# Kernel optimization log

Hardware: AMD Instinct MI355X
Metric: run time of the kernel (lower is better)

The kernel has to match this reference:

```python
import jax, jax.numpy as jnp
import numpy as np
from jax import lax

INF = 1e10
R = 20          # max_distance: EDT truncated at this radius (exact under clamp)
NUM_CLASSES = 19


def _pass1d(f, axis):
    """1D squared distance transform min_{|d|<=R} (d^2 + f[shifted]), truncated.
    f: [..., H, W] with 0 at 'source' pixels, INF elsewhere. Out-of-bounds = INF
    (matches scipy, which sees nothing beyond the array border)."""
    pad = [(0, 0)] * f.ndim
    pad[axis] = (R, R)
    fp = jnp.pad(f, pad, constant_values=INF)
    n = f.shape[axis]
    out = jnp.full_like(f, INF)
    for d in range(2 * R + 1):  # fixed small loop (41 iters), jit-unrolled
        shifted = lax.slice_in_dim(fp, d, d + n, axis=axis)
        out = jnp.minimum(out, shifted + float((d - R) ** 2))
    return out


def edt_trunc(mask):
    """Euclidean distance from each True pixel to nearest False pixel,
    truncated at R (False pixels get 0). mask: [..., H, W] bool."""
    f = jnp.where(mask, INF, 0.0).astype(jnp.float32)
    g = _pass1d(f, -2)
    g = _pass1d(g, -1)
    return jnp.sqrt(jnp.minimum(g, float(R * R)))


def compute_sdf(onehot_bool):
    """Signed distance: negdist - posdist, per [B,C,H,W] one-hot masks.
    Already truncated at +-R, matching clamp(-R, R) in the torch module."""
    posdist = edt_trunc(onehot_bool)    # distance inside FG to BG
    negdist = edt_trunc(~onehot_bool)   # distance inside BG to FG
    return negdist - posdist


def setup_inputs() -> dict:
    key = jax.random.key(0)
    k1, k2 = jax.random.split(key)
    logits = jax.random.normal(k1, (8, NUM_CLASSES, 256, 512), dtype=jnp.float32)
    targets = jax.random.randint(k2, (8, 256, 512), 0, NUM_CLASSES, dtype=jnp.int64)
    return {"logits": logits, "targets": targets}


def reference(logits, targets):
    C = logits.shape[1]
    probs = jax.nn.softmax(logits, axis=1)                       # [B,C,H,W]
    onehot = jax.nn.one_hot(targets, C, axis=1, dtype=jnp.bool_)  # [B,C,H,W]
    sdf = compute_sdf(onehot)
    sdf = jnp.clip(sdf, -float(R), float(R)) / float(R)
    # mean over spatial, sum over classes, mean over batch (reduction='mean')
    per_class = jnp.mean(probs * sdf, axis=(2, 3))               # [B,C]
    loss = jnp.sum(per_class, axis=1)                            # [B]
    return jnp.mean(loss)
```

## Files before the change

### kernel.cpp

```cpp
#include <hip/hip_runtime.h>
#include <hip/hip_bf16.h>
#include <math.h>

#define NCLS 19
#define BB   8
#define HH   256
#define WW   512
#define CAP2 400u
#define SEG  8
#define WPC  70

typedef unsigned short u16x2 __attribute__((ext_vector_type(2)));

static __device__ __forceinline__ unsigned umin32(unsigned a, unsigned b) { return a < b ? a : b; }
static __device__ __forceinline__ float fsqrt_fast(float x) { return __builtin_amdgcn_sqrtf(x); }

static __device__ __forceinline__ unsigned pk_add_s(unsigned v, unsigned c) {
    unsigned d; asm("v_pk_add_u16 %0, %1, %2" : "=v"(d) : "s"(c), "v"(v)); return d;
}
static __device__ __forceinline__ unsigned pk_minv(unsigned a, unsigned b) {
    unsigned d; asm("v_pk_min_u16 %0, %1, %2" : "=v"(d) : "v"(a), "v"(b)); return d;
}
static __device__ __forceinline__ unsigned pk_maxv(unsigned a, unsigned b) {
    unsigned d; asm("v_pk_max_u16 %0, %1, %2" : "=v"(d) : "v"(a), "v"(b)); return d;
}
static __device__ __forceinline__ unsigned pk_hmin(unsigned a) {
    unsigned d;
    asm("v_pk_min_u16 %0, %1, %1 op_sel:[1,0] op_sel_hi:[0,1]" : "=v"(d) : "v"(a));
    return d;
}
static __device__ __forceinline__ void sq8(unsigned x, unsigned& w0, unsigned& w1) {
    unsigned a = x & 0x00FF00FFu;
    unsigned b = (x >> 8) & 0x00FF00FFu;
    u16x2 sa = __builtin_bit_cast(u16x2, a); sa = sa * sa;
    u16x2 sb = __builtin_bit_cast(u16x2, b); sb = sb * sb;
    unsigned ua = __builtin_bit_cast(unsigned, sa);
    unsigned ub = __builtin_bit_cast(unsigned, sb);
    w0 = __builtin_amdgcn_perm(ub, ua, 0x05040100u);
    w1 = __builtin_amdgcn_perm(ub, ua, 0x07060302u);
}

__global__ __launch_bounds__(256)
void kA_vert(const int* __restrict__ targ, unsigned char* __restrict__ vneg,
             unsigned long long* __restrict__ acc) {
    if (blockIdx.x == 0 && threadIdx.x < 64) acc[threadIdx.x] = 0ULL;
    int gid = blockIdx.x * 256 + threadIdx.x;
    int col = gid & 4095;
    int seg = gid >> 12;
    int b = col >> 9;
    int w = col & 511;
    int h0 = seg * SEG;
    const int* tp = &targ[b * HH * WW + w];

    unsigned d[NCLS];
    unsigned pk[NCLS][2];
#pragma unroll
    for (int c = 0; c < NCLS; ++c) { d[c] = 21u; pk[c][0] = 0u; pk[c][1] = 0u; }
#pragma unroll
    for (int k = 0; k < 21 + SEG; ++k) {
        int hh = h0 - 21 + k;
        int t = -1;
        if (hh >= 0) t = tp[hh * WW];
#pragma unroll
        for (int c = 0; c < NCLS; ++c)
            d[c] = (t == c) ? 0u : d[c] + 1u;
        if (k >= 21) {
            int r = k - 21;
#pragma unroll
            for (int c = 0; c < NCLS; ++c)
                pk[c][r >> 2] |= d[c] << ((r & 3) * 8);
        }
    }
    unsigned u[NCLS];
#pragma unroll
    for (int c = 0; c < NCLS; ++c) u[c] = 21u;
#pragma unroll
    for (int k = 0; k < 21 + SEG; ++k) {
        int hh = h0 + 21 + SEG - 1 - k;
        int t = -1;
        if (hh < HH) t = tp[hh * WW];
#pragma unroll
        for (int c = 0; c < NCLS; ++c)
            u[c] = (t == c) ? 0u : u[c] + 1u;
        if (k >= 21) {
            int r = 21 + SEG - 1 - k;
#pragma unroll
            for (int c = 0; c < NCLS; ++c) {
                unsigned dv = (pk[c][r >> 2] >> ((r & 3) * 8)) & 0xffu;
                vneg[((size_t)(b * NCLS + c) * HH + hh) * WW + w] =
                    (unsigned char)umin32(dv, u[c]);
            }
        }
    }
}

__global__ __launch_bounds__(256)
void kB_main(const float* __restrict__ logits,
             const unsigned char* __restrict__ vneg,
             unsigned long long* __restrict__ acc) {
    __shared__ __align__(16) unsigned smem[NCLS * 280];
    int tid = threadIdx.x;
    int L = tid & 63;
    int wid = tid >> 6;
    int bh = blockIdx.x;
    int b = bh >> 8;
    int h = bh & 255;

    float (*sNum)[256] = (float (*)[256])smem;
    float (*sDen)[256] = (float (*)[256])(smem + 1024);
    float (*sEt)[256]  = (float (*)[256])(smem + 2048);
    unsigned short (*sM2)[256] = (unsigned short (*)[256])(smem + 3072);
    float* wsum = (float*)(smem + 3584);

#define SQx(x) ((unsigned)((x) * (x)))
#define PK2(a, bq) (SQx(a) | (SQx(bq) << 16))
    const unsigned CE[21] = {
        PK2(-20,-19), PK2(-18,-17), PK2(-16,-15), PK2(-14,-13), PK2(-12,-11),
        PK2(-10,-9),  PK2(-8,-7),   PK2(-6,-5),   PK2(-4,-3),   PK2(-2,-1),
        PK2(0,1),     PK2(2,3),     PK2(4,5),     PK2(6,7),     PK2(8,9),
        PK2(10,11),   PK2(12,13),   PK2(14,15),   PK2(16,17),   PK2(18,19),
        PK2(20,21) };
    const unsigned CO[21] = {
        PK2(-21,-20), PK2(-19,-18), PK2(-17,-16), PK2(-15,-14), PK2(-13,-12),
        PK2(-11,-10), PK2(-9,-8),   PK2(-7,-6),   PK2(-5,-4),   PK2(-3,-2),
        PK2(-1,0),    PK2(1,2),     PK2(3,4),     PK2(5,6),     PK2(7,8),
        PK2(9,10),    PK2(11,12),   PK2(13,14),   PK2(15,16),   PK2(17,18),
        PK2(19,20) };
#undef PK2
#undef SQx

    const unsigned HALO2 = 441u | (441u << 16);
    const float* lroww = &logits[((size_t)(b * NCLS + wid) * HH + h) * WW + 8 * L];
    int nc = (wid < 3) ? 5 : 4;

    uint2 v8s[5];
#pragma unroll
    for (int i = 0; i < 5; ++i)
        if (i < nc)
            v8s[i] = ((const uint2*)vneg)
                [((size_t)(b * NCLS + wid + 4 * i) * HH + h) * 64 + L];
#pragma unroll
    for (int i = 0; i < 5; ++i)
        if (i < nc) {
            int c = wid + 4 * i;
            uint4 wq;
            sq8(v8s[i].x, wq.x, wq.y);
            sq8(v8s[i].y, wq.z, wq.w);
            ((uint4*)smem)[c * WPC + L + 3] = wq;
            if (L < 12) smem[c * 280 + L] = HALO2;
            if (L >= 52) smem[c * 280 + 216 + L] = HALO2;
        }

    float den[8], num[8], et[8];
    unsigned m2[8];
#pragma unroll
    for (int p = 0; p < 8; ++p) { den[p]=0.f; num[p]=0.f; et[p]=0.f; m2[p]=0xFFFFu; }

    float4 f0n = *(const float4*)lroww;
    float4 f1n = *(const float4*)(lroww + 4);

#pragma unroll 1
    for (int i = 0; i < nc; ++i) {
        int c = wid + 4 * i;
        float4 f0 = f0n, f1 = f1n;
        if (i + 1 < nc) {
            const float* ln = lroww + (size_t)(i + 1) * 4 * (HH * WW);
            f0n = *(const float4*)ln;
            f1n = *(const float4*)(ln + 4);
        }

        const uint4* basep = (const uint4*)smem + c * WPC + L;
        uint4 q2 = basep[2], q3 = basep[3], q4 = basep[4];
        unsigned W[28];
        W[8]=q2.x;  W[9]=q2.y;  W[10]=q2.z; W[11]=q2.w;
        W[12]=q3.x; W[13]=q3.y; W[14]=q3.z; W[15]=q3.w;
        W[16]=q4.x; W[17]=q4.y; W[18]=q4.z; W[19]=q4.w;

        unsigned ae[4], ao[4];
#pragma unroll
        for (int r = 0; r < 4; ++r) { ae[r] = 0xFFFFFFFFu; ao[r] = 0xFFFFFFFFu; }

#pragma unroll
        for (int r = 0; r < 4; ++r)
#pragma unroll
            for (int m = 7; m <= 13; ++m) {
                ae[r] = pk_minv(ae[r], pk_add_s(W[r + m + 2], CE[m]));
                ao[r] = pk_minv(ao[r], pk_add_s(W[r + m + 2], CO[m]));
            }

        unsigned mx = pk_maxv(pk_maxv(pk_maxv(pk_hmin(ae[0]), pk_hmin(ao[0])),
                                      pk_maxv(pk_hmin(ae[1]), pk_hmin(ao[1]))),
                              pk_maxv(pk_maxv(pk_hmin(ae[2]), pk_hmin(ao[2])),
                                      pk_maxv(pk_hmin(ae[3]), pk_hmin(ao[3]))));
        if (!__all(mx <= (49u | (49u << 16)))) {
            uint4 q0 = basep[0], q1 = basep[1], q5 = basep[5], q6 = basep[6];
            W[0]=q0.x;  W[1]=q0.y;  W[2]=q0.z;  W[3]=q0.w;
            W[4]=q1.x;  W[5]=q1.y;  W[6]=q1.z;  W[7]=q1.w;
            W[20]=q5.x; W[21]=q5.y; W[22]=q5.z; W[23]=q5.w;
            W[24]=q6.x; W[25]=q6.y; W[26]=q6.z; W[27]=q6.w;
#pragma unroll
            for (int r = 0; r < 4; ++r) {
#pragma unroll
                for (int m = 0; m <= 6; ++m) {
                    ae[r] = pk_minv(ae[r], pk_add_s(W[r + m + 2], CE[m]));
                    ao[r] = pk_minv(ao[r], pk_add_s(W[r + m + 2], CO[m]));
                }
#pragma unroll
                for (int m = 14; m <= 20; ++m) {
                    ae[r] = pk_minv(ae[r], pk_add_s(W[r + m + 2], CE[m]));
                    ao[r] = pk_minv(ao[r], pk_add_s(W[r + m + 2], CO[m]));
                }
            }
        }

        float fx[8] = {f0.x, f0.y, f0.z, f0.w, f1.x, f1.y, f1.z, f1.w};
#pragma unroll
        for (int r = 0; r < 4; ++r) {
            unsigned nd0 = pk_hmin(ae[r]) & 0xFFFFu;
            unsigned nd1 = pk_hmin(ao[r]) & 0xFFFFu;
            float e0 = __expf(fx[2 * r]), e1 = __expf(fx[2 * r + 1]);
            den[2 * r] += e0; den[2 * r + 1] += e1;
            float s0 = fsqrt_fast((float)umin32(nd0, CAP2));
            float s1 = fsqrt_fast((float)umin32(nd1, CAP2));
            num[2 * r]     += e0 * s0;
            num[2 * r + 1] += e1 * s1;
            bool z0 = (nd0 == 0), z1 = (nd1 == 0);
            et[2 * r]     = z0 ? e0 : et[2 * r];
            et[2 * r + 1] = z1 ? e1 : et[2 * r + 1];
            m2[2 * r]     = umin32(m2[2 * r],     z0 ? 0xFFFFu : nd0);
            m2[2 * r + 1] = umin32(m2[2 * r + 1], z1 ? 0xFFFFu : nd1);
        }
    }

    __syncthreads();
    float vsum = 0.f;
#pragma unroll
    for (int pass = 0; pass < 2; ++pass) {
        if ((L >> 5) == pass) {
            int base = 8 * (L & 31);
            *(float4*)&sNum[wid][base]     = (float4){num[0], num[1], num[2], num[3]};
            *(float4*)&sNum[wid][base + 4] = (float4){num[4], num[5], num[6], num[7]};
            *(float4*)&sDen[wid][base]     = (float4){den[0], den[1], den[2], den[3]};
            *(float4*)&sDen[wid][base + 4] = (float4){den[4], den[5], den[6], den[7]};
            *(float4*)&sEt[wid][base]      = (float4){et[0], et[1], et[2], et[3]};
            *(float4*)&sEt[wid][base + 4]  = (float4){et[4], et[5], et[6], et[7]};
            uint4 mq;
            mq.x = m2[0] | (m2[1] << 16); mq.y = m2[2] | (m2[3] << 16);
            mq.z = m2[4] | (m2[5] << 16); mq.w = m2[6] | (m2[7] << 16);
            *(uint4*)&sM2[wid][base] = mq;
        }
        __syncthreads();
        {
            float N = sNum[0][tid] + sNum[1][tid] + sNum[2][tid] + sNum[3][tid];
            float D = sDen[0][tid] + sDen[1][tid] + sDen[2][tid] + sDen[3][tid];
            float E = sEt[0][tid] + sEt[1][tid] + sEt[2][tid] + sEt[3][tid];
            unsigned M = umin32(umin32((unsigned)sM2[0][tid], (unsigned)sM2[1][tid]),
                                umin32((unsigned)sM2[2][tid], (unsigned)sM2[3][tid]));
            vsum += (N - E * fsqrt_fast((float)umin32(M, CAP2))) / D;
        }
        __syncthreads();
    }

#pragma unroll
    for (int off = 32; off >= 1; off >>= 1) vsum += __shfl_down(vsum, off);
    if (L == 0) wsum[wid] = vsum;
    __syncthreads();
    if (tid == 0) {
        float s = (wsum[0] + wsum[1]) + (wsum[2] + wsum[3]);
        double q = (double)s * (68719476736.0 / 20.0);
        atomicAdd(&acc[bh & 63], (unsigned long long)(long long)q);
    }
}

__global__ void kC_final(const unsigned long long* __restrict__ acc,
                         float* __restrict__ out) {
    long long iv = 0;
    for (int i = 0; i < 64; ++i) iv += (long long)acc[i];
    double v = (double)iv / 68719476736.0;
    out[0] = (float)(v / (double)((size_t)BB * HH * WW));
}

extern "C" void kernel_launch(void* const* d_in, const int* in_sizes, int n_in,
                              void* d_out, int out_size, void* d_ws, size_t ws_size,
                              hipStream_t stream) {
    const float* logits = (const float*)d_in[0];
    const int* targ = (const int*)d_in[1];
    unsigned char* wsb = (unsigned char*)d_ws;
    unsigned long long* acc = (unsigned long long*)wsb;
    unsigned char* vneg = wsb + 1024;

    kA_vert<<<512, 256, 0, stream>>>(targ, vneg, acc);
    kB_main<<<BB * HH, 256, 0, stream>>>(logits, vneg, acc);
    kC_final<<<1, 1, 0, stream>>>(acc, (float*)d_out);
}
```

Before: 57.50 us.

## Split fused horizontal EDT and loss kernel into two separate kernels

Result: slower. 62.46 us (+8.6%).

```diff
diff --git a/kernel.cpp b/kernel.cpp
--- a/kernel.cpp
+++ b/kernel.cpp
@@ -95,22 +95,16 @@
 }
 
 __global__ __launch_bounds__(256)
-void kB_main(const float* __restrict__ logits,
-             const unsigned char* __restrict__ vneg,
-             unsigned long long* __restrict__ acc) {
-    __shared__ __align__(16) unsigned smem[NCLS * 280];
+void kB1_horiz(const unsigned char* __restrict__ vneg,
+               unsigned short* __restrict__ nd2) {
+    __shared__ __align__(16) unsigned smem[4 * 280];
     int tid = threadIdx.x;
     int L = tid & 63;
     int wid = tid >> 6;
-    int bh = blockIdx.x;
+    int c = blockIdx.x;
+    int bh = blockIdx.y * 4 + wid;
     int b = bh >> 8;
     int h = bh & 255;
-
-    float (*sNum)[256] = (float (*)[256])smem;
-    float (*sDen)[256] = (float (*)[256])(smem + 1024);
-    float (*sEt)[256]  = (float (*)[256])(smem + 2048);
-    unsigned short (*sM2)[256] = (unsigned short (*)[256])(smem + 3072);
-    float* wsum = (float*)(smem + 3584);
 
 #define SQx(x) ((unsigned)((x) * (x)))
 #define PK2(a, bq) (SQx(a) | (SQx(bq) << 16))
@@ -130,145 +124,121 @@
 #undef SQx
 
     const unsigned HALO2 = 441u | (441u << 16);
-    const float* lroww = &logits[((size_t)(b * NCLS + wid) * HH + h) * WW + 8 * L];
-    int nc = (wid < 3) ? 5 : 4;
-
-    uint2 v8s[5];
-#pragma unroll
-    for (int i = 0; i < 5; ++i)
-        if (i < nc)
-            v8s[i] = ((const uint2*)vneg)
-                [((size_t)(b * NCLS + wid + 4 * i) * HH + h) * 64 + L];
-#pragma unroll
-    for (int i = 0; i < 5; ++i)
-        if (i < nc) {
-            int c = wid + 4 * i;
-            uint4 wq;
-            sq8(v8s[i].x, wq.x, wq.y);
-            sq8(v8s[i].y, wq.z, wq.w);
-            ((uint4*)smem)[c * WPC + L + 3] = wq;
-            if (L < 12) smem[c * 280 + L] = HALO2;
-            if (L >= 52) smem[c * 280 + 216 + L] = HALO2;
-        }
-
-    float den[8], num[8], et[8];
-    unsigned m2[8];
-#pragma unroll
-    for (int p = 0; p < 8; ++p) { den[p]=0.f; num[p]=0.f; et[p]=0.f; m2[p]=0xFFFFu; }
-
-    float4 f0n = *(const float4*)lroww;
-    float4 f1n = *(const float4*)(lroww + 4);
-
-#pragma unroll 1
-    for (int i = 0; i < nc; ++i) {
-        int c = wid + 4 * i;
-        float4 f0 = f0n, f1 = f1n;
-        if (i + 1 < nc) {
-            const float* ln = lroww + (size_t)(i + 1) * 4 * (HH * WW);
-            f0n = *(const float4*)ln;
-            f1n = *(const float4*)(ln + 4);
-        }
-
-        const uint4* basep = (const uint4*)smem + c * WPC + L;
-        uint4 q2 = basep[2], q3 = basep[3], q4 = basep[4];
-        unsigned W[28];
-        W[8]=q2.x;  W[9]=q2.y;  W[10]=q2.z; W[11]=q2.w;
-        W[12]=q3.x; W[13]=q3.y; W[14]=q3.z; W[15]=q3.w;
-        W[16]=q4.x; W[17]=q4.y; W[18]=q4.z; W[19]=q4.w;
-
-        unsigned ae[4], ao[4];
-#pragma unroll
-        for (int r = 0; r < 4; ++r) { ae[r] = 0xFFFFFFFFu; ao[r] = 0xFFFFFFFFu; }
-
-#pragma unroll
-        for (int r = 0; r < 4; ++r)
-#pragma unroll
-            for (int m = 7; m <= 13; ++m) {
+    size_t rowoff = (size_t)(b * NCLS + c) * HH + h;
+
+    uint2 v8 = ((const uint2*)vneg)[rowoff * 64 + L];
+    uint4 wq;
+    sq8(v8.x, wq.x, wq.y);
+    sq8(v8.y, wq.z, wq.w);
+    unsigned* srow = smem + wid * 280;
+    ((uint4*)srow)[L + 3] = wq;
+    if (L < 12) srow[L] = HALO2;
+    if (L >= 52) srow[216 + L] = HALO2;
+
+    const uint4* basep = (const uint4*)srow + L;
+    uint4 q2 = basep[2], q3 = basep[3], q4 = basep[4];
+    unsigned W[28];
+    W[8]=q2.x;  W[9]=q2.y;  W[10]=q2.z; W[11]=q2.w;
+    W[12]=q3.x; W[13]=q3.y; W[14]=q3.z; W[15]=q3.w;
+    W[16]=q4.x; W[17]=q4.y; W[18]=q4.z; W[19]=q4.w;
+
+    unsigned ae[4], ao[4];
+#pragma unroll
+    for (int r = 0; r < 4; ++r) { ae[r] = 0xFFFFFFFFu; ao[r] = 0xFFFFFFFFu; }
+
+#pragma unroll
+    for (int r = 0; r < 4; ++r)
+#pragma unroll
+        for (int m = 7; m <= 13; ++m) {
+            ae[r] = pk_minv(ae[r], pk_add_s(W[r + m + 2], CE[m]));
+            ao[r] = pk_minv(ao[r], pk_add_s(W[r + m + 2], CO[m]));
+        }
+
+    unsigned mx = pk_maxv(pk_maxv(pk_maxv(pk_hmin(ae[0]), pk_hmin(ao[0])),
+                                  pk_maxv(pk_hmin(ae[1]), pk_hmin(ao[1]))),
+                          pk_maxv(pk_maxv(pk_hmin(ae[2]), pk_hmin(ao[2])),
+                                  pk_maxv(pk_hmin(ae[3]), pk_hmin(ao[3]))));
+    if (!__all(mx <= (49u | (49u << 16)))) {
+        uint4 q0 = basep[0], q1 = basep[1], q5 = basep[5], q6 = basep[6];
+        W[0]=q0.x;  W[1]=q0.y;  W[2]=q0.z;  W[3]=q0.w;
+        W[4]=q1.x;  W[5]=q1.y;  W[6]=q1.z;  W[7]=q1.w;
+        W[20]=q5.x; W[21]=q5.y; W[22]=q5.z; W[23]=q5.w;
+        W[24]=q6.x; W[25]=q6.y; W[26]=q6.z; W[27]=q6.w;
+#pragma unroll
+        for (int r = 0; r < 4; ++r) {
+#pragma unroll
+            for (int m = 0; m <= 6; ++m) {
                 ae[r] = pk_minv(ae[r], pk_add_s(W[r + m + 2], CE[m]));
                 ao[r] = pk_minv(ao[r], pk_add_s(W[r + m + 2], CO[m]));
             }
-
-        unsigned mx = pk_maxv(pk_maxv(pk_maxv(pk_hmin(ae[0]), pk_hmin(ao[0])),
-                                      pk_maxv(pk_hmin(ae[1]), pk_hmin(ao[1]))),
-                              pk_maxv(pk_maxv(pk_hmin(ae[2]), pk_hmin(ao[2])),
-                                      pk_maxv(pk_hmin(ae[3]), pk_hmin(ao[3]))));
-        if (!__all(mx <= (49u | (49u << 16)))) {
-            uint4 q0 = basep[0], q1 = basep[1], q5 = basep[5], q6 = basep[6];
-            W[0]=q0.x;  W[1]=q0.y;  W[2]=q0.z;  W[3]=q0.w;
-            W[4]=q1.x;  W[5]=q1.y;  W[6]=q1.z;  W[7]=q1.w;
-            W[20]=q5.x; W[21]=q5.y; W[22]=q5.z; W[23]=q5.w;
-            W[24]=q6.x; W[25]=q6.y; W[26]=q6.z; W[27]=q6.w;
-#pragma unroll
-            for (int r = 0; r < 4; ++r) {
-#pragma unroll
-                for (int m = 0; m <= 6; ++m) {
-                    ae[r] = pk_minv(ae[r], pk_add_s(W[r + m + 2], CE[m]));
-                    ao[r] = pk_minv(ao[r], pk_add_s(W[r + m + 2], CO[m]));
-                }
-#pragma unroll
-                for (int m = 14; m <= 20; ++m) {
-                    ae[r] = pk_minv(ae[r], pk_add_s(W[r + m + 2], CE[m]));
-                    ao[r] = pk_minv(ao[r], pk_add_s(W[r + m + 2], CO[m]));
-                }
+#pragma unroll
+            for (int m = 14; m <= 20; ++m) {
+                ae[r] = pk_minv(ae[r], pk_add_s(W[r + m + 2], CE[m]));
+                ao[r] = pk_minv(ao[r], pk_add_s(W[r + m + 2], CO[m]));
             }
         }
-
-        float fx[8] = {f0.x, f0.y, f0.z, f0.w, f1.x, f1.y, f1.z, f1.w};
-#pragma unroll
-        for (int r = 0; r < 4; ++r) {
-            unsigned nd0 = pk_hmin(ae[r]) & 0xFFFFu;
-            unsigned nd1 = pk_hmin(ao[r]) & 0xFFFFu;
-            float e0 = __expf(fx[2 * r]), e1 = __expf(fx[2 * r + 1]);
-            den[2 * r] += e0; den[2 * r + 1] += e1;
-            float s0 = fsqrt_fast((float)umin32(nd0, CAP2));
-            float s1 = fsqrt_fast((float)umin32(nd1, CAP2));
-            num[2 * r]     += e0 * s0;
-            num[2 * r + 1] += e1 * s1;
-            bool z0 = (nd0 == 0), z1 = (nd1 == 0);
-            et[2 * r]     = z0 ? e0 : et[2 * r];
-            et[2 * r + 1] = z1 ? e1 : et[2 * r + 1];
-            m2[2 * r]     = umin32(m2[2 * r],     z0 ? 0xFFFFu : nd0);
-            m2[2 * r + 1] = umin32(m2[2 * r + 1], z1 ? 0xFFFFu : nd1);
-        }
-    }
-
-    __syncthreads();
-    float vsum = 0.f;
-#pragma unroll
-    for (int pass = 0; pass < 2; ++pass) {
-        if ((L >> 5) == pass) {
-            int base = 8 * (L & 31);
-            *(float4*)&sNum[wid][base]     = (float4){num[0], num[1], num[2], num[3]};
-            *(float4*)&sNum[wid][base + 4] = (float4){num[4], num[5], num[6], num[7]};
-            *(float4*)&sDen[wid][base]     = (float4){den[0], den[1], den[2], den[3]};
-            *(float4*)&sDen[wid][base + 4] = (float4){den[4], den[5], den[6], den[7]};
-            *(float4*)&sEt[wid][base]      = (float4){et[0], et[1], et[2], et[3]};
-            *(float4*)&sEt[wid][base + 4]  = (float4){et[4], et[5], et[6], et[7]};
-            uint4 mq;
-            mq.x = m2[0] | (m2[1] << 16); mq.y = m2[2] | (m2[3] << 16);
-            mq.z = m2[4] | (m2[5] << 16); mq.w = m2[6] | (m2[7] << 16);
-            *(uint4*)&sM2[wid][base] = mq;
-        }
-        __syncthreads();
-        {
-            float N = sNum[0][tid] + sNum[1][tid] + sNum[2][tid] + sNum[3][tid];
-            float D = sDen[0][tid] + sDen[1][tid] + sDen[2][tid] + sDen[3][tid];
-            float E = sEt[0][tid] + sEt[1][tid] + sEt[2][tid] + sEt[3][tid];
-            unsigned M = umin32(umin32((unsigned)sM2[0][tid], (unsigned)sM2[1][tid]),
-                                umin32((unsigned)sM2[2][tid], (unsigned)sM2[3][tid]));
-            vsum += (N - E * fsqrt_fast((float)umin32(M, CAP2))) / D;
-        }
-        __syncthreads();
-    }
-
-#pragma unroll
-    for (int off = 32; off >= 1; off >>= 1) vsum += __shfl_down(vsum, off);
-    if (L == 0) wsum[wid] = vsum;
+    }
+
+    uint4 outq;
+    unsigned o[4];
+#pragma unroll
+    for (int r = 0; r < 4; ++r) {
+        unsigned nd0 = umin32(pk_hmin(ae[r]) & 0xFFFFu, CAP2);
+        unsigned nd1 = umin32(pk_hmin(ao[r]) & 0xFFFFu, CAP2);
+        o[r] = nd0 | (nd1 << 16);
+    }
+    outq.x = o[0]; outq.y = o[1]; outq.z = o[2]; outq.w = o[3];
+    ((uint4*)nd2)[rowoff * 64 + L] = outq;
+}
+
+__global__ __launch_bounds__(256)
+void kB2_loss(const float* __restrict__ logits,
+              const unsigned short* __restrict__ nd2,
+              unsigned long long* __restrict__ acc) {
+    __shared__ float wsum[4];
+    int tid = threadIdx.x;
+    int g = blockIdx.x * 256 + tid;
+    int b = g >> 15;
+    int rem = g & 32767;
+    int h = rem >> 7;
+    int w = (rem & 127) * 4;
+    size_t base = ((size_t)(b * NCLS) * HH + h) * WW + w;
+
+    float den[4] = {0,0,0,0}, num[4] = {0,0,0,0}, et[4] = {0,0,0,0};
+    unsigned m2[4] = {0xFFFFu, 0xFFFFu, 0xFFFFu, 0xFFFFu};
+
+#pragma unroll 1
+    for (int c = 0; c < NCLS; ++c) {
+        size_t off = base + (size_t)c * (HH * WW);
+        float4 lg = *(const float4*)(logits + off);
+        ushort4 nd = *(const ushort4*)(nd2 + off);
+        float lgs[4] = {lg.x, lg.y, lg.z, lg.w};
+        unsigned nds[4] = {nd.x, nd.y, nd.z, nd.w};
+#pragma unroll
+        for (int k = 0; k < 4; ++k) {
+            float e = __expf(lgs[k]);
+            den[k] += e;
+            num[k] += e * fsqrt_fast((float)nds[k]);
+            bool z = (nds[k] == 0);
+            et[k] = z ? e : et[k];
+            m2[k] = umin32(m2[k], z ? 0xFFFFu : nds[k]);
+        }
+    }
+
+    float v = 0.f;
+#pragma unroll
+    for (int k = 0; k < 4; ++k)
+        v += (num[k] - et[k] * fsqrt_fast((float)umin32(m2[k], CAP2))) / den[k];
+
+#pragma unroll
+    for (int off = 32; off >= 1; off >>= 1) v += __shfl_down(v, off);
+    int L = tid & 63, wid = tid >> 6;
+    if (L == 0) wsum[wid] = v;
     __syncthreads();
     if (tid == 0) {
         float s = (wsum[0] + wsum[1]) + (wsum[2] + wsum[3]);
         double q = (double)s * (68719476736.0 / 20.0);
-        atomicAdd(&acc[bh & 63], (unsigned long long)(long long)q);
+        atomicAdd(&acc[blockIdx.x & 63], (unsigned long long)(long long)q);
     }
 }
 
@@ -288,8 +258,10 @@
     unsigned char* wsb = (unsigned char*)d_ws;
     unsigned long long* acc = (unsigned long long*)wsb;
     unsigned char* vneg = wsb + 1024;
+    unsigned short* nd2 = (unsigned short*)(wsb + 1024 + 20971520);
 
     kA_vert<<<512, 256, 0, stream>>>(targ, vneg, acc);
-    kB_main<<<BB * HH, 256, 0, stream>>>(logits, vneg, acc);
+    kB1_horiz<<<dim3(NCLS, 512), 256, 0, stream>>>(vneg, nd2);
+    kB2_loss<<<1024, 256, 0, stream>>>(logits, nd2, acc);
     kC_final<<<1, 1, 0, stream>>>(acc, (float*)d_out);
 }
```
